# Optimization experiments

Measured on AMD Instinct MI355X. Metric: run time of the kernel, lower is better.

The kernel has to match this reference:

```python
import jax, jax.numpy as jnp
import numpy as np

B, TQ, TK, D, H = 4, 2048, 2048, 512, 8
NEG = -1e9
LN_EPS = 1e-3  # Keras LayerNormalization default


def setup_inputs() -> dict:
    key = jax.random.key(0)
    ks = jax.random.split(key, 5)
    s = 0.02
    return {
        "queries": jax.random.normal(ks[0], (B, TQ, D), jnp.float32),
        "keys_in": jax.random.normal(ks[1], (B, TK, D), jnp.float32),
        "Wq": jax.random.normal(ks[2], (D, D), jnp.float32) * s,
        "bq": jnp.zeros((D,), jnp.float32),
        "Wk": jax.random.normal(ks[3], (D, D), jnp.float32) * s,
        "bk": jnp.zeros((D,), jnp.float32),
        "Wv": jax.random.normal(ks[4], (D, D), jnp.float32) * s,
        "bv": jnp.zeros((D,), jnp.float32),
        "gamma": jnp.ones((D,), jnp.float32),
        "beta": jnp.zeros((D,), jnp.float32),
    }


def reference(queries, keys_in, Wq, bq, Wk, bk, Wv, bv, gamma, beta):
    # Dense projections with relu activation (as in the original layer)
    Q = jax.nn.relu(queries @ Wq + bq)   # [B, Tq, D]
    K = jax.nn.relu(keys_in @ Wk + bk)   # [B, Tk, D]
    V = jax.nn.relu(keys_in @ Wv + bv)   # [B, Tk, D]

    b, tq, d = Q.shape
    tk = K.shape[1]
    dh = d // H
    # split_heads: tf.split(axis=-1)+concat(axis=0) == contiguous feature chunks per head
    Qh = Q.reshape(b, tq, H, dh)
    Kh = K.reshape(b, tk, H, dh)
    Vh = V.reshape(b, tk, H, dh)

    scores = jnp.einsum('bqhd,bkhd->bhqk', Qh, Kh) / jnp.sqrt(jnp.float32(dh))

    # key padding mask derived from per-head K content: sum(|K|) > 0 along dh
    kmask = jnp.sum(jnp.abs(Kh), axis=-1) > 0            # [B, Tk, H]
    kmask = jnp.transpose(kmask, (0, 2, 1))              # [B, H, Tk]
    scores = jnp.where(kmask[:, :, None, :], scores, NEG)

    attn = jax.nn.softmax(scores, axis=-1)               # [B, H, Tq, Tk]

    # query mask: zero out attention rows for all-zero query positions
    qmask = (jnp.sum(jnp.abs(Qh), axis=-1) > 0).astype(attn.dtype)  # [B, Tq, H]
    qmask = jnp.transpose(qmask, (0, 2, 1))              # [B, H, Tq]
    attn = attn * qmask[:, :, :, None]

    out = jnp.einsum('bhqk,bkhd->bqhd', attn, Vh).reshape(b, tq, d)

    # residual + LayerNorm (Keras default: last axis, eps=1e-3)
    res = out + queries
    mu = jnp.mean(res, axis=-1, keepdims=True)
    var = jnp.var(res, axis=-1, keepdims=True)
    return (res - mu) * jax.lax.rsqrt(var + LN_EPS) * gamma + beta
```

## Files before the change

### kernel.cpp

```cpp
#include <hip/hip_runtime.h>
#include <cstdint>

#define BB 4
#define TT 2048
#define DD 512
#define HH 8
#define DH 64
#define NT (TT / 64)
#define LOG2E 1.4426950408889634f

using bf16x8 = __attribute__((ext_vector_type(8))) __bf16;
using f32x4  = __attribute__((ext_vector_type(4))) float;
using f32x16 = __attribute__((ext_vector_type(16))) float;
using us8    = __attribute__((ext_vector_type(8))) unsigned short;
using us4    = __attribute__((ext_vector_type(4))) unsigned short;
using u32x2  = __attribute__((ext_vector_type(2))) unsigned int;

typedef const __attribute__((address_space(1))) unsigned int* as1cp;
typedef __attribute__((address_space(3))) unsigned int* as3p;

__device__ __forceinline__ void gload16(const void* g, void* l) {
  __builtin_amdgcn_global_load_lds((as1cp)(uintptr_t)g,
                                   (as3p)(unsigned int)(uintptr_t)l, 16, 0, 0);
}

__device__ __forceinline__ unsigned short f2bf(float x) {
  unsigned int u = __float_as_uint(x);
  u += 0x7fffu + ((u >> 16) & 1u);
  return (unsigned short)(u >> 16);
}
__device__ __forceinline__ float bf2f(unsigned short u) {
  return __uint_as_float(((unsigned int)u) << 16);
}
__device__ __forceinline__ f32x4 MFMA(bf16x8 a, bf16x8 b, f32x4 c) {
  return __builtin_amdgcn_mfma_f32_16x16x32_bf16(a, b, c, 0, 0, 0);
}
__device__ __forceinline__ f32x16 MFMA32(bf16x8 a, bf16x8 b, f32x16 c) {
  return __builtin_amdgcn_mfma_f32_32x32x16_bf16(a, b, c, 0, 0, 0);
}

#define WAITVM(N) asm volatile("s_waitcnt vmcnt(" #N ")" ::: "memory")
#define RAWBAR() asm volatile("s_barrier" ::: "memory")

__global__ __launch_bounds__(256) void prep_kernel(const float4* __restrict__ q,
                                                   const float4* __restrict__ k,
                                                   us4* __restrict__ qb,
                                                   us4* __restrict__ kb,
                                                   const float* __restrict__ Wq,
                                                   const float* __restrict__ Wk,
                                                   const float* __restrict__ Wv,
                                                   unsigned short* __restrict__ Wt) {
  __shared__ float tile[32][33];
  int id = blockIdx.x;
  if (id < 4096) {
    size_t i = (size_t)id * 256 + threadIdx.x;
    float4 a = q[i];
    us4 o; o[0] = f2bf(a.x); o[1] = f2bf(a.y); o[2] = f2bf(a.z); o[3] = f2bf(a.w);
    qb[i] = o;
    float4 b = k[i];
    us4 p; p[0] = f2bf(b.x); p[1] = f2bf(b.y); p[2] = f2bf(b.z); p[3] = f2bf(b.w);
    kb[i] = p;
  } else {
    int id2 = id - 4096;
    int z = id2 >> 8, rem = id2 & 255;
    const float* W = (z == 0) ? Wq : (z == 1) ? Wk : Wv;
    int k0 = (rem & 15) * 32, n0 = (rem >> 4) * 32;
    int r = threadIdx.x >> 5, c = threadIdx.x & 31;
#pragma unroll
    for (int p = 0; p < 4; ++p)
      tile[r + p * 8][c] = W[(size_t)(k0 + r + p * 8) * DD + n0 + c];
    __syncthreads();
    unsigned short* o = Wt + (size_t)z * DD * DD;
#pragma unroll
    for (int p = 0; p < 4; ++p)
      o[(size_t)(n0 + r + p * 8) * DD + k0 + c] = f2bf(tile[c][r + p * 8]);
  }
}

#define GSTAGE(kt2, pbuf)                                                    \
  {                                                                          \
    int t_ = threadIdx.x;                                                    \
    _Pragma("unroll")                                                        \
    for (int it_ = 0; it_ < 2; ++it_) {                                      \
      int c_ = t_ + it_ * 256;                                               \
      gload16(A  + (size_t)(mb + (c_ >> 2)) * DD + (kt2) * 32 + (c_ & 3) * 8,\
              &As[pbuf][(size_t)c_ * 8]);                                    \
      gload16(Bt + (size_t)(nb + (c_ >> 2)) * DD + (kt2) * 32 + (c_ & 3) * 8,\
              &Bs[pbuf][(size_t)c_ * 8]);                                    \
    }                                                                        \
  }

__global__ __launch_bounds__(256) void gemm_proj(const unsigned short* __restrict__ qb,
                                                 const unsigned short* __restrict__ kb,
                                                 const unsigned short* __restrict__ Wt,
                                                 const float* __restrict__ bq,
                                                 const float* __restrict__ bk,
                                                 const float* __restrict__ bv,
                                                 unsigned short* __restrict__ Qp,
                                                 unsigned short* __restrict__ Kp,
                                                 unsigned short* __restrict__ Vp,
                                                 float* __restrict__ qmask,
                                                 uint2* __restrict__ kbits) {
  int z = blockIdx.z;
  const unsigned short* A  = (z == 0) ? qb : kb;
  const unsigned short* Bt = Wt + (size_t)z * DD * DD;
  const float* bias = (z == 0) ? bq : (z == 1) ? bk : bv;
  unsigned short* out = (z == 0) ? Qp : (z == 1) ? Kp : Vp;
  const float osc = (z == 0) ? 0.125f * LOG2E : 1.0f;

  __shared__ __align__(16) unsigned short As[2][128 * 32];
  __shared__ __align__(16) unsigned short Bs[2][128 * 32];

  int mb = blockIdx.x * 128, nb = blockIdx.y * 128;
  int w = threadIdx.x >> 6, lane = threadIdx.x & 63;
  int l15 = lane & 15, lg = lane >> 4;
  int wr = (w >> 1) * 64, wc = (w & 1) * 64;

  f32x4 acc[4][4] = {};

  GSTAGE(0, 0);
  for (int kt = 0; kt < DD / 32; ++kt) {
    int pb2 = kt & 1;
    if (kt + 1 < DD / 32) {
      GSTAGE(kt + 1, pb2 ^ 1);
      WAITVM(4);
    } else {
      WAITVM(0);
    }
    RAWBAR();

    bf16x8 af[4], bf[4];
#pragma unroll
    for (int m = 0; m < 4; ++m)
      af[m] = *(const bf16x8*)&As[pb2][(wr + m * 16 + l15) * 32 + lg * 8];
#pragma unroll
    for (int n = 0; n < 4; ++n)
      bf[n] = *(const bf16x8*)&Bs[pb2][(wc + n * 16 + l15) * 32 + lg * 8];
#pragma unroll
    for (int m = 0; m < 4; ++m)
#pragma unroll
      for (int n = 0; n < 4; ++n)
        acc[m][n] = MFMA(af[m], bf[n], acc[m][n]);

    if (kt + 1 < DD / 32) RAWBAR();
  }

  float rs_[16];
#pragma unroll
  for (int j = 0; j < 16; ++j) rs_[j] = 0.f;
#pragma unroll
  for (int m = 0; m < 4; ++m)
#pragma unroll
    for (int n = 0; n < 4; ++n)
#pragma unroll
      for (int i = 0; i < 4; ++i) {
        int row = mb + wr + m * 16 + lg * 4 + i;
        int col = nb + wc + n * 16 + l15;
        float v = fmaxf(acc[m][n][i] + bias[col], 0.f);
        rs_[m * 4 + i] += v;
        out[(size_t)row * DD + col] = f2bf(v * osc);
      }

  if (z < 2) {
#pragma unroll
    for (int j = 0; j < 16; ++j) {
      rs_[j] += __shfl_xor(rs_[j], 1);
      rs_[j] += __shfl_xor(rs_[j], 2);
      rs_[j] += __shfl_xor(rs_[j], 4);
      rs_[j] += __shfl_xor(rs_[j], 8);
    }
    int gr0 = mb + wr;
    int b = gr0 >> 11, tpos0 = gr0 & (TT - 1);
    int h = (nb + wc) >> 6;
    int bh = b * HH + h;
    if (z == 0) {
      if (l15 == 0) {
#pragma unroll
        for (int m = 0; m < 4; ++m)
#pragma unroll
          for (int i = 0; i < 4; ++i) {
            int tpos = tpos0 + m * 16 + lg * 4 + i;
            qmask[(size_t)bh * TT + tpos] = (rs_[m * 4 + i] > 0.f) ? 1.f : 0.f;
          }
      }
    } else {
      unsigned long long wloc = 0;
#pragma unroll
      for (int m = 0; m < 4; ++m)
#pragma unroll
        for (int i = 0; i < 4; ++i)
          if (rs_[m * 4 + i] > 0.f)
            wloc |= 1ull << (m * 16 + lg * 4 + i);
      wloc |= __shfl_xor(wloc, 16);
      wloc |= __shfl_xor(wloc, 32);
      if (lane == 0)
        kbits[bh * NT + (tpos0 >> 6)] =
            make_uint2((unsigned int)wloc, (unsigned int)(wloc >> 32));
    }
  }
}

__global__ __launch_bounds__(256) void post_v(const unsigned short* __restrict__ Vp,
                                              unsigned short* __restrict__ Vt) {
  __shared__ unsigned short tile[64][72];
  int id = blockIdx.x;
  int b = id >> 8, k0 = (id & 31) * 64, d0 = ((id >> 5) & 7) * 64;
  int t = threadIdx.x;
  int r = t >> 3, c8 = (t & 7) * 8;
#pragma unroll
  for (int p = 0; p < 2; ++p) {
    int row = r + p * 32;
    us8 v = *(const us8*)&Vp[(size_t)(b * TT + k0 + row) * DD + d0 + c8];
#pragma unroll
    for (int j = 0; j < 8; ++j) tile[row][c8 + j] = v[j];
  }
  __syncthreads();
#pragma unroll
  for (int p = 0; p < 2; ++p) {
    int dr = r + p * 32;
    us8 o;
#pragma unroll
    for (int j = 0; j < 8; ++j) o[j] = tile[c8 + j][dr];
    *(us8*)&Vt[((size_t)b * DD + d0 + dr) * TT + k0 + c8] = o;
  }
}

#define STAGE(tt, pbuf)                                                      \
  {                                                                          \
    int c0_ = threadIdx.x;                                                   \
    _Pragma("unroll")                                                        \
    for (int it_ = 0; it_ < 2; ++it_) {                                      \
      int c_ = c0_ + it_ * 256;                                              \
      int r_ = c_ >> 3, j_ = c_ & 7;                                         \
      int js_ = j_ ^ (r_ & 7);                                               \
      int kr_ = (r_ & ~12) | ((r_ & 4) << 1) | ((r_ & 8) >> 1);              \
      gload16(kg + (size_t)((tt) * 64 + kr_) * DD + js_ * 8,                 \
              &KsBuf[pbuf][(size_t)c_ * 8]);                                 \
      gload16(vg + (size_t)r_ * TT + (tt) * 64 + js_ * 8,                    \
              &VsBuf[pbuf][(size_t)c_ * 8]);                                 \
    }                                                                        \
  }

__global__ __launch_bounds__(256) void attn_kernel(
    const unsigned short* __restrict__ Qp,
    const unsigned short* __restrict__ Kp,
    const unsigned short* __restrict__ Vt,
    const uint2* __restrict__ kbits,
    const float* __restrict__ qmask,
    unsigned short* __restrict__ O) {
  __shared__ __align__(16) unsigned short KsBuf[2][64 * 64];
  __shared__ __align__(16) unsigned short VsBuf[2][64 * 64];

  const int w = threadIdx.x >> 6;
  const int lane = threadIdx.x & 63;
  const int l31 = lane & 31, h2 = lane >> 5;

  int flat = blockIdx.x;
  int wg = (flat & 7) * 64 + (flat >> 3);
  int qt = wg & 15, bh = wg >> 4;
  int h = bh & 7, b = bh >> 3;
  int q0 = qt * 128 + w * 32;

  const unsigned short* qbase =
      Qp + ((size_t)(b * TT + q0 + l31)) * DD + h * DH + h2 * 8;
  bf16x8 qf[4];
#pragma unroll
  for (int kd = 0; kd < 4; ++kd) qf[kd] = *(const bf16x8*)(qbase + kd * 16);

  const unsigned short* kg = Kp + ((size_t)b * TT) * DD + h * DH;
  const unsigned short* vg = Vt + ((size_t)(b * DD + h * DH)) * TT;
  const uint2* kb_ptr = kbits + (size_t)bh * NT;

  f32x16 oat0 = {}, oat1 = {};
  float l_i = 0.f;

  STAGE(0, 0);

  for (int t = 0; t < NT; ++t) {
    int pb = t & 1;
    if (t + 1 < NT) {
      STAGE(t + 1, pb ^ 1);
      WAITVM(4);
    } else {
      WAITVM(0);
    }
    RAWBAR();

    const unsigned short* ksb = &KsBuf[pb][0];
    const unsigned short* vsb = &VsBuf[pb][0];

    bf16x8 kf0[4], kf1[4];
#pragma unroll
    for (int kd = 0; kd < 4; ++kd) {
      int x = ((kd * 2 + h2) ^ (l31 & 7)) << 3;
      kf0[kd] = *(const bf16x8*)&ksb[l31 * 64 + x];
      kf1[kd] = *(const bf16x8*)&ksb[(32 + l31) * 64 + x];
    }
    f32x16 s0 = {}, s1 = {};
    __builtin_amdgcn_s_setprio(1);
#pragma unroll
    for (int kd = 0; kd < 4; ++kd) s0 = MFMA32(kf0[kd], qf[kd], s0);
#pragma unroll
    for (int kd = 0; kd < 4; ++kd) s1 = MFMA32(kf1[kd], qf[kd], s1);
    __builtin_amdgcn_s_setprio(0);

    bf16x8 vf0[4], vf1[4];
#pragma unroll
    for (int ks = 0; ks < 4; ++ks) {
      int x = ((ks * 2 + h2) ^ (l31 & 7)) << 3;
      vf0[ks] = *(const bf16x8*)&vsb[l31 * 64 + x];
      vf1[ks] = *(const bf16x8*)&vsb[(32 + l31) * 64 + x];
    }

    uint2 kw = kb_ptr[t];
    if ((kw.x & kw.y) != 0xffffffffu) {
#pragma unroll
      for (int r = 0; r < 16; ++r) {
        int sh = ((r >> 3) << 4) + (h2 << 3) + (r & 7);
        if (!((kw.x >> sh) & 1)) s0[r] = -1e30f;
        if (!((kw.y >> sh) & 1)) s1[r] = -1e30f;
      }
    }

    float a0 = 0.f, a1 = 0.f, a2 = 0.f, a3 = 0.f;
#pragma unroll
    for (int r = 0; r < 8; ++r)  { float p = exp2f(s0[r]); s0[r] = p; a0 += p; }
#pragma unroll
    for (int r = 8; r < 16; ++r) { float p = exp2f(s0[r]); s0[r] = p; a1 += p; }
#pragma unroll
    for (int r = 0; r < 8; ++r)  { float p = exp2f(s1[r]); s1[r] = p; a2 += p; }
#pragma unroll
    for (int r = 8; r < 16; ++r) { float p = exp2f(s1[r]); s1[r] = p; a3 += p; }
    l_i += (a0 + a1) + (a2 + a3);

    bf16x8 pbf[4];
#pragma unroll
    for (int j = 0; j < 8; ++j) {
      pbf[0][j] = (__bf16)s0[j];
      pbf[1][j] = (__bf16)s0[8 + j];
      pbf[2][j] = (__bf16)s1[j];
      pbf[3][j] = (__bf16)s1[8 + j];
    }

    __builtin_amdgcn_s_setprio(1);
#pragma unroll
    for (int ks = 0; ks < 4; ++ks) {
      oat0 = MFMA32(vf0[ks], pbf[ks], oat0);
      oat1 = MFMA32(vf1[ks], pbf[ks], oat1);
    }
    __builtin_amdgcn_s_setprio(0);

    if (t + 1 < NT) RAWBAR();
  }

  u32x2 sr = __builtin_amdgcn_permlane32_swap(__float_as_uint(l_i),
                                              __float_as_uint(l_i), false, false);
  float l = __uint_as_float(sr[0]) + __uint_as_float(sr[1]);
  float qm = qmask[(size_t)bh * TT + q0 + l31];
  float sc = qm / fmaxf(l, 1e-30f);
  unsigned short* ob = O + ((size_t)(b * TT + q0 + l31)) * DD + h * DH + h2 * 4;
#pragma unroll
  for (int qq = 0; qq < 4; ++qq) {
    us4 w0, w1;
#pragma unroll
    for (int i = 0; i < 4; ++i) {
      w0[i] = f2bf(oat0[4 * qq + i] * sc);
      w1[i] = f2bf(oat1[4 * qq + i] * sc);
    }
    *(us4*)(ob + 8 * qq) = w0;
    *(us4*)(ob + 32 + 8 * qq) = w1;
  }
}

__global__ __launch_bounds__(256) void ln_kernel(const unsigned short* __restrict__ O,
                                                 const float* __restrict__ qin,
                                                 const float* __restrict__ gamma,
                                                 const float* __restrict__ beta,
                                                 float* __restrict__ out) {
  int row = blockIdx.x * 4 + (threadIdx.x >> 6);
  int lane = threadIdx.x & 63;
  size_t base = (size_t)row * DD + lane * 8;
  us8 o = *(const us8*)(O + base);
  const float4* q4 = (const float4*)(qin + base);
  float4 c = q4[0], d2 = q4[1];
  float qv[8] = {c.x, c.y, c.z, c.w, d2.x, d2.y, d2.z, d2.w};
  float v[8];
#pragma unroll
  for (int j = 0; j < 8; ++j) v[j] = bf2f(o[j]) + qv[j];
  float s = 0.f, s2 = 0.f;
#pragma unroll
  for (int j = 0; j < 8; ++j) { s += v[j]; s2 += v[j] * v[j]; }
#pragma unroll
  for (int xm = 1; xm < 64; xm <<= 1) {
    s += __shfl_xor(s, xm);
    s2 += __shfl_xor(s2, xm);
  }
  float mu = s * (1.0f / DD);
  float var = s2 * (1.0f / DD) - mu * mu;
  float rs = rsqrtf(var + 1e-3f);
  const float* g = gamma + lane * 8;
  const float* bb = beta + lane * 8;
  float* ob = out + base;
#pragma unroll
  for (int j = 0; j < 8; ++j) ob[j] = (v[j] - mu) * rs * g[j] + bb[j];
}

extern "C" void kernel_launch(void* const* d_in, const int* in_sizes, int n_in,
                              void* d_out, int out_size, void* d_ws, size_t ws_size,
                              hipStream_t stream) {
  (void)in_sizes; (void)n_in; (void)out_size; (void)ws_size;
  const float* queries = (const float*)d_in[0];
  const float* keys_in = (const float*)d_in[1];
  const float* Wq = (const float*)d_in[2];
  const float* bq = (const float*)d_in[3];
  const float* Wk = (const float*)d_in[4];
  const float* bk = (const float*)d_in[5];
  const float* Wv = (const float*)d_in[6];
  const float* bv = (const float*)d_in[7];
  const float* gamma = (const float*)d_in[8];
  const float* beta  = (const float*)d_in[9];
  float* out = (float*)d_out;

  char* ws = (char*)d_ws;
  unsigned short* qb = (unsigned short*)(ws);
  unsigned short* kb = (unsigned short*)(ws + (8ull << 20));
  unsigned short* Obf = (unsigned short*)(ws);
  unsigned short* Qp = (unsigned short*)(ws + (16ull << 20));
  unsigned short* Kp = (unsigned short*)(ws + (24ull << 20));
  unsigned short* Vp = (unsigned short*)(ws + (32ull << 20));
  unsigned short* Vt = (unsigned short*)(ws + (40ull << 20));
  unsigned short* Wt = (unsigned short*)(ws + (48ull << 20));
  float* qmaskp = (float*)(ws + (50ull << 20));
  uint2* kbitsp = (uint2*)(ws + (50ull << 20) + (512ull << 10));

  prep_kernel<<<4864, 256, 0, stream>>>((const float4*)queries, (const float4*)keys_in,
                                        (us4*)qb, (us4*)kb, Wq, Wk, Wv, Wt);
  gemm_proj<<<dim3(64, 4, 3), 256, 0, stream>>>(qb, kb, Wt, bq, bk, bv,
                                                Qp, Kp, Vp, qmaskp, kbitsp);
  post_v<<<1024, 256, 0, stream>>>(Vp, Vt);
  attn_kernel<<<512, 256, 0, stream>>>(Qp, Kp, Vt, kbitsp, qmaskp, Obf);
  ln_kernel<<<2048, 256, 0, stream>>>(Obf, queries, gamma, beta, out);
}
```

Measured before the change: 195.0 us.

## Fuse fp32-to-bf16 conversion and V transpose into projection GEMM, unroll attention loop

The projection GEMM now loads fp32 activations straight into LDS and converts them to bf16 while building fragments. This removes the separate activation conversion pass and its intermediate buffers. The V projection epilogue writes transposed bf16 directly, which removes the post_v kernel. The attention loop is unrolled by two with pointer increments, and the softmax row sum is computed with an MFMA against a ones vector instead of scalar adds. In exchange, the GEMM uses twice the LDS for the A tile and does more conversion work per fragment, and the transposed V stores are strided 8-byte writes.

```diff
diff --git a/kernel.cpp b/kernel.cpp
--- a/kernel.cpp
+++ b/kernel.cpp
@@ -42,73 +42,61 @@
 #define WAITVM(N) asm volatile("s_waitcnt vmcnt(" #N ")" ::: "memory")
 #define RAWBAR() asm volatile("s_barrier" ::: "memory")
 
-__global__ __launch_bounds__(256) void prep_kernel(const float4* __restrict__ q,
-                                                   const float4* __restrict__ k,
-                                                   us4* __restrict__ qb,
-                                                   us4* __restrict__ kb,
-                                                   const float* __restrict__ Wq,
-                                                   const float* __restrict__ Wk,
-                                                   const float* __restrict__ Wv,
-                                                   unsigned short* __restrict__ Wt) {
+__global__ __launch_bounds__(256) void prep_w(const float* __restrict__ Wq,
+                                              const float* __restrict__ Wk,
+                                              const float* __restrict__ Wv,
+                                              unsigned short* __restrict__ Wt) {
   __shared__ float tile[32][33];
   int id = blockIdx.x;
-  if (id < 4096) {
-    size_t i = (size_t)id * 256 + threadIdx.x;
-    float4 a = q[i];
-    us4 o; o[0] = f2bf(a.x); o[1] = f2bf(a.y); o[2] = f2bf(a.z); o[3] = f2bf(a.w);
-    qb[i] = o;
-    float4 b = k[i];
-    us4 p; p[0] = f2bf(b.x); p[1] = f2bf(b.y); p[2] = f2bf(b.z); p[3] = f2bf(b.w);
-    kb[i] = p;
-  } else {
-    int id2 = id - 4096;
-    int z = id2 >> 8, rem = id2 & 255;
-    const float* W = (z == 0) ? Wq : (z == 1) ? Wk : Wv;
-    int k0 = (rem & 15) * 32, n0 = (rem >> 4) * 32;
-    int r = threadIdx.x >> 5, c = threadIdx.x & 31;
-#pragma unroll
-    for (int p = 0; p < 4; ++p)
-      tile[r + p * 8][c] = W[(size_t)(k0 + r + p * 8) * DD + n0 + c];
-    __syncthreads();
-    unsigned short* o = Wt + (size_t)z * DD * DD;
-#pragma unroll
-    for (int p = 0; p < 4; ++p)
-      o[(size_t)(n0 + r + p * 8) * DD + k0 + c] = f2bf(tile[c][r + p * 8]);
-  }
-}
-
-#define GSTAGE(kt2, pbuf)                                                    \
-  {                                                                          \
-    int t_ = threadIdx.x;                                                    \
-    _Pragma("unroll")                                                        \
-    for (int it_ = 0; it_ < 2; ++it_) {                                      \
-      int c_ = t_ + it_ * 256;                                               \
-      gload16(A  + (size_t)(mb + (c_ >> 2)) * DD + (kt2) * 32 + (c_ & 3) * 8,\
-              &As[pbuf][(size_t)c_ * 8]);                                    \
-      gload16(Bt + (size_t)(nb + (c_ >> 2)) * DD + (kt2) * 32 + (c_ & 3) * 8,\
-              &Bs[pbuf][(size_t)c_ * 8]);                                    \
-    }                                                                        \
-  }
-
-__global__ __launch_bounds__(256) void gemm_proj(const unsigned short* __restrict__ qb,
-                                                 const unsigned short* __restrict__ kb,
+  int z = id >> 8, rem = id & 255;
+  const float* W = (z == 0) ? Wq : (z == 1) ? Wk : Wv;
+  int k0 = (rem & 15) * 32, n0 = (rem >> 4) * 32;
+  int r = threadIdx.x >> 5, c = threadIdx.x & 31;
+#pragma unroll
+  for (int p = 0; p < 4; ++p)
+    tile[r + p * 8][c] = W[(size_t)(k0 + r + p * 8) * DD + n0 + c];
+  __syncthreads();
+  unsigned short* o = Wt + (size_t)z * DD * DD;
+#pragma unroll
+  for (int p = 0; p < 4; ++p)
+    o[(size_t)(n0 + r + p * 8) * DD + k0 + c] = f2bf(tile[c][r + p * 8]);
+}
+
+#define GSTAGE(kt2, pbuf)                                                     \
+  {                                                                           \
+    int t_ = threadIdx.x;                                                     \
+    _Pragma("unroll")                                                         \
+    for (int it_ = 0; it_ < 4; ++it_) {                                       \
+      int c_ = t_ + it_ * 256;             \
+      gload16(A + (size_t)(mb + (c_ >> 3)) * DD + (kt2) * 32 + (c_ & 7) * 4,  \
+              &Asf[pbuf][(size_t)c_ * 4]);                                    \
+    }                                                                         \
+    _Pragma("unroll")                                                         \
+    for (int it_ = 0; it_ < 2; ++it_) {                                       \
+      int c_ = t_ + it_ * 256;             \
+      gload16(Bt + (size_t)(nb + (c_ >> 2)) * DD + (kt2) * 32 + (c_ & 3) * 8, \
+              &Bs[pbuf][(size_t)c_ * 8]);                                     \
+    }                                                                         \
+  }
+
+__global__ __launch_bounds__(256) void gemm_proj(const float* __restrict__ queries,
+                                                 const float* __restrict__ keys_in,
                                                  const unsigned short* __restrict__ Wt,
                                                  const float* __restrict__ bq,
                                                  const float* __restrict__ bk,
                                                  const float* __restrict__ bv,
                                                  unsigned short* __restrict__ Qp,
                                                  unsigned short* __restrict__ Kp,
-                                                 unsigned short* __restrict__ Vp,
+                                                 unsigned short* __restrict__ Vt,
                                                  float* __restrict__ qmask,
                                                  uint2* __restrict__ kbits) {
   int z = blockIdx.z;
-  const unsigned short* A  = (z == 0) ? qb : kb;
+  const float* A = (z == 0) ? queries : keys_in;
   const unsigned short* Bt = Wt + (size_t)z * DD * DD;
   const float* bias = (z == 0) ? bq : (z == 1) ? bk : bv;
-  unsigned short* out = (z == 0) ? Qp : (z == 1) ? Kp : Vp;
   const float osc = (z == 0) ? 0.125f * LOG2E : 1.0f;
 
-  __shared__ __align__(16) unsigned short As[2][128 * 32];
+  __shared__ __align__(16) float Asf[2][128 * 32];
   __shared__ __align__(16) unsigned short Bs[2][128 * 32];
 
   int mb = blockIdx.x * 128, nb = blockIdx.y * 128;
@@ -123,7 +111,7 @@
     int pb2 = kt & 1;
     if (kt + 1 < DD / 32) {
       GSTAGE(kt + 1, pb2 ^ 1);
-      WAITVM(4);
+      WAITVM(6);
     } else {
       WAITVM(0);
     }
@@ -131,8 +119,16 @@
 
     bf16x8 af[4], bf[4];
 #pragma unroll
-    for (int m = 0; m < 4; ++m)
-      af[m] = *(const bf16x8*)&As[pb2][(wr + m * 16 + l15) * 32 + lg * 8];
+    for (int m = 0; m < 4; ++m) {
+      int base = (wr + m * 16 + l15) * 32 + lg * 8;
+      f32x4 lo = *(const f32x4*)&Asf[pb2][base];
+      f32x4 hi = *(const f32x4*)&Asf[pb2][base + 4];
+#pragma unroll
+      for (int j = 0; j < 4; ++j) {
+        af[m][j] = (__bf16)lo[j];
+        af[m][4 + j] = (__bf16)hi[j];
+      }
+    }
 #pragma unroll
     for (int n = 0; n < 4; ++n)
       bf[n] = *(const bf16x8*)&Bs[pb2][(wc + n * 16 + l15) * 32 + lg * 8];
@@ -148,20 +144,21 @@
   float rs_[16];
 #pragma unroll
   for (int j = 0; j < 16; ++j) rs_[j] = 0.f;
-#pragma unroll
-  for (int m = 0; m < 4; ++m)
-#pragma unroll
-    for (int n = 0; n < 4; ++n)
-#pragma unroll
-      for (int i = 0; i < 4; ++i) {
-        int row = mb + wr + m * 16 + lg * 4 + i;
-        int col = nb + wc + n * 16 + l15;
-        float v = fmaxf(acc[m][n][i] + bias[col], 0.f);
-        rs_[m * 4 + i] += v;
-        out[(size_t)row * DD + col] = f2bf(v * osc);
-      }
 
   if (z < 2) {
+    unsigned short* out = (z == 0) ? Qp : Kp;
+#pragma unroll
+    for (int m = 0; m < 4; ++m)
+#pragma unroll
+      for (int n = 0; n < 4; ++n)
+#pragma unroll
+        for (int i = 0; i < 4; ++i) {
+          int row = mb + wr + m * 16 + lg * 4 + i;
+          int col = nb + wc + n * 16 + l15;
+          float v = fmaxf(acc[m][n][i] + bias[col], 0.f);
+          rs_[m * 4 + i] += v;
+          out[(size_t)row * DD + col] = f2bf(v * osc);
+        }
 #pragma unroll
     for (int j = 0; j < 16; ++j) {
       rs_[j] += __shfl_xor(rs_[j], 1);
@@ -197,35 +194,24 @@
         kbits[bh * NT + (tpos0 >> 6)] =
             make_uint2((unsigned int)wloc, (unsigned int)(wloc >> 32));
     }
-  }
-}
-
-__global__ __launch_bounds__(256) void post_v(const unsigned short* __restrict__ Vp,
-                                              unsigned short* __restrict__ Vt) {
-  __shared__ unsigned short tile[64][72];
-  int id = blockIdx.x;
-  int b = id >> 8, k0 = (id & 31) * 64, d0 = ((id >> 5) & 7) * 64;
-  int t = threadIdx.x;
-  int r = t >> 3, c8 = (t & 7) * 8;
-#pragma unroll
-  for (int p = 0; p < 2; ++p) {
-    int row = r + p * 32;
-    us8 v = *(const us8*)&Vp[(size_t)(b * TT + k0 + row) * DD + d0 + c8];
-#pragma unroll
-    for (int j = 0; j < 8; ++j) tile[row][c8 + j] = v[j];
-  }
-  __syncthreads();
-#pragma unroll
-  for (int p = 0; p < 2; ++p) {
-    int dr = r + p * 32;
-    us8 o;
-#pragma unroll
-    for (int j = 0; j < 8; ++j) o[j] = tile[c8 + j][dr];
-    *(us8*)&Vt[((size_t)b * DD + d0 + dr) * TT + k0 + c8] = o;
-  }
-}
-
-#define STAGE(tt, pbuf)                                                      \
+  } else {
+    int b = mb >> 11;
+    int tok0 = (mb & (TT - 1)) + wr + lg * 4;
+#pragma unroll
+    for (int m = 0; m < 4; ++m)
+#pragma unroll
+      for (int n = 0; n < 4; ++n) {
+        int col = nb + wc + n * 16 + l15;
+        us4 pk;
+#pragma unroll
+        for (int i = 0; i < 4; ++i)
+          pk[i] = f2bf(fmaxf(acc[m][n][i] + bias[col], 0.f));
+        *(us4*)&Vt[((size_t)b * DD + col) * TT + tok0 + m * 16] = pk;
+      }
+  }
+}
+
+#define STAGE(kgt, vgt, pbuf)                                                \
   {                                                                          \
     int c0_ = threadIdx.x;                                                   \
     _Pragma("unroll")                                                        \
@@ -234,11 +220,79 @@
       int r_ = c_ >> 3, j_ = c_ & 7;                                         \
       int js_ = j_ ^ (r_ & 7);                                               \
       int kr_ = (r_ & ~12) | ((r_ & 4) << 1) | ((r_ & 8) >> 1);              \
-      gload16(kg + (size_t)((tt) * 64 + kr_) * DD + js_ * 8,                 \
+      gload16((kgt) + (size_t)kr_ * DD + js_ * 8,                            \
               &KsBuf[pbuf][(size_t)c_ * 8]);                                 \
-      gload16(vg + (size_t)r_ * TT + (tt) * 64 + js_ * 8,                    \
+      gload16((vgt) + (size_t)r_ * TT + js_ * 8,                             \
               &VsBuf[pbuf][(size_t)c_ * 8]);                                 \
     }                                                                        \
+  }
+
+#define ATTN_TILE(pbuf, do_stage)                                            \
+  {                                                                          \
+    if (do_stage) {                                                          \
+      STAGE(kgt, vgt, pbuf ^ 1);                                             \
+      kgt += 64 * DD;                                                        \
+      vgt += 64;                                                             \
+      WAITVM(4);                                                             \
+    } else {                                                                 \
+      WAITVM(0);                                                             \
+    }                                                                        \
+    RAWBAR();                                                                \
+    const unsigned short* ksb = &KsBuf[pbuf][0];                             \
+    const unsigned short* vsb = &VsBuf[pbuf][0];                             \
+    bf16x8 kf0[4], kf1[4];                                                   \
+    _Pragma("unroll")                                                        \
+    for (int kd = 0; kd < 4; ++kd) {                                         \
+      int x = ((kd * 2 + h2) ^ (l31 & 7)) << 3;                              \
+      kf0[kd] = *(const bf16x8*)&ksb[l31 * 64 + x];                          \
+      kf1[kd] = *(const bf16x8*)&ksb[(32 + l31) * 64 + x];                   \
+    }                                                                        \
+    f32x16 s0 = {}, s1 = {};                                                 \
+    __builtin_amdgcn_s_setprio(1);                                           \
+    _Pragma("unroll")                                                        \
+    for (int kd = 0; kd < 4; ++kd) s0 = MFMA32(kf0[kd], qf[kd], s0);         \
+    _Pragma("unroll")                                                        \
+    for (int kd = 0; kd < 4; ++kd) s1 = MFMA32(kf1[kd], qf[kd], s1);         \
+    __builtin_amdgcn_s_setprio(0);                                           \
+    bf16x8 vf0[4], vf1[4];                                                   \
+    _Pragma("unroll")                                                        \
+    for (int ks = 0; ks < 4; ++ks) {                                         \
+      int x = ((ks * 2 + h2) ^ (l31 & 7)) << 3;                              \
+      vf0[ks] = *(const bf16x8*)&vsb[l31 * 64 + x];                          \
+      vf1[ks] = *(const bf16x8*)&vsb[(32 + l31) * 64 + x];                   \
+    }                                                                        \
+    uint2 kw = *kbt;                                                         \
+    ++kbt;                                                                   \
+    if ((kw.x & kw.y) != 0xffffffffu) {                                      \
+      _Pragma("unroll")                                                      \
+      for (int r = 0; r < 16; ++r) {                                         \
+        int sh = ((r >> 3) << 4) + (h2 << 3) + (r & 7);                      \
+        if (!((kw.x >> sh) & 1)) s0[r] = -1e30f;                             \
+        if (!((kw.y >> sh) & 1)) s1[r] = -1e30f;                             \
+      }                                                                      \
+    }                                                                        \
+    _Pragma("unroll")                                                        \
+    for (int r = 0; r < 16; ++r) {                                           \
+      s0[r] = exp2f(s0[r]);                                                  \
+      s1[r] = exp2f(s1[r]);                                                  \
+    }                                                                        \
+    bf16x8 pbf[4];                                                           \
+    _Pragma("unroll")                                                        \
+    for (int j = 0; j < 8; ++j) {                                            \
+      pbf[0][j] = (__bf16)s0[j];                                             \
+      pbf[1][j] = (__bf16)s0[8 + j];                                         \
+      pbf[2][j] = (__bf16)s1[j];                                             \
+      pbf[3][j] = (__bf16)s1[8 + j];                                         \
+    }                                                                        \
+    __builtin_amdgcn_s_setprio(1);                                           \
+    _Pragma("unroll")                                                        \
+    for (int ks = 0; ks < 4; ++ks) {                                         \
+      oat0 = MFMA32(vf0[ks], pbf[ks], oat0);                                 \
+      oat1 = MFMA32(vf1[ks], pbf[ks], oat1);                                 \
+      lacc = MFMA32(ones, pbf[ks], lacc);                                    \
+    }                                                                        \
+    __builtin_amdgcn_s_setprio(0);                                           \
+    if (do_stage) RAWBAR();                                                  \
   }
 
 __global__ __launch_bounds__(256) void attn_kernel(
@@ -267,92 +321,29 @@
 #pragma unroll
   for (int kd = 0; kd < 4; ++kd) qf[kd] = *(const bf16x8*)(qbase + kd * 16);
 
-  const unsigned short* kg = Kp + ((size_t)b * TT) * DD + h * DH;
-  const unsigned short* vg = Vt + ((size_t)(b * DD + h * DH)) * TT;
-  const uint2* kb_ptr = kbits + (size_t)bh * NT;
-
-  f32x16 oat0 = {}, oat1 = {};
-  float l_i = 0.f;
-
-  STAGE(0, 0);
-
-  for (int t = 0; t < NT; ++t) {
-    int pb = t & 1;
-    if (t + 1 < NT) {
-      STAGE(t + 1, pb ^ 1);
-      WAITVM(4);
-    } else {
-      WAITVM(0);
-    }
-    RAWBAR();
-
-    const unsigned short* ksb = &KsBuf[pb][0];
-    const unsigned short* vsb = &VsBuf[pb][0];
-
-    bf16x8 kf0[4], kf1[4];
-#pragma unroll
-    for (int kd = 0; kd < 4; ++kd) {
-      int x = ((kd * 2 + h2) ^ (l31 & 7)) << 3;
-      kf0[kd] = *(const bf16x8*)&ksb[l31 * 64 + x];
-      kf1[kd] = *(const bf16x8*)&ksb[(32 + l31) * 64 + x];
-    }
-    f32x16 s0 = {}, s1 = {};
-    __builtin_amdgcn_s_setprio(1);
-#pragma unroll
-    for (int kd = 0; kd < 4; ++kd) s0 = MFMA32(kf0[kd], qf[kd], s0);
-#pragma unroll
-    for (int kd = 0; kd < 4; ++kd) s1 = MFMA32(kf1[kd], qf[kd], s1);
-    __builtin_amdgcn_s_setprio(0);
-
-    bf16x8 vf0[4], vf1[4];
-#pragma unroll
-    for (int ks = 0; ks < 4; ++ks) {
-      int x = ((ks * 2 + h2) ^ (l31 & 7)) << 3;
-      vf0[ks] = *(const bf16x8*)&vsb[l31 * 64 + x];
-      vf1[ks] = *(const bf16x8*)&vsb[(32 + l31) * 64 + x];
-    }
-
-    uint2 kw = kb_ptr[t];
-    if ((kw.x & kw.y) != 0xffffffffu) {
-#pragma unroll
-      for (int r = 0; r < 16; ++r) {
-        int sh = ((r >> 3) << 4) + (h2 << 3) + (r & 7);
-        if (!((kw.x >> sh) & 1)) s0[r] = -1e30f;
-        if (!((kw.y >> sh) & 1)) s1[r] = -1e30f;
-      }
-    }
-
-    float a0 = 0.f, a1 = 0.f, a2 = 0.f, a3 = 0.f;
-#pragma unroll
-    for (int r = 0; r < 8; ++r)  { float p = exp2f(s0[r]); s0[r] = p; a0 += p; }
-#pragma unroll
-    for (int r = 8; r < 16; ++r) { float p = exp2f(s0[r]); s0[r] = p; a1 += p; }
-#pragma unroll
-    for (int r = 0; r < 8; ++r)  { float p = exp2f(s1[r]); s1[r] = p; a2 += p; }
-#pragma unroll
-    for (int r = 8; r < 16; ++r) { float p = exp2f(s1[r]); s1[r] = p; a3 += p; }
-    l_i += (a0 + a1) + (a2 + a3);
-
-    bf16x8 pbf[4];
-#pragma unroll
-    for (int j = 0; j < 8; ++j) {
-      pbf[0][j] = (__bf16)s0[j];
-      pbf[1][j] = (__bf16)s0[8 + j];
-      pbf[2][j] = (__bf16)s1[j];
-      pbf[3][j] = (__bf16)s1[8 + j];
-    }
-
-    __builtin_amdgcn_s_setprio(1);
-#pragma unroll
-    for (int ks = 0; ks < 4; ++ks) {
-      oat0 = MFMA32(vf0[ks], pbf[ks], oat0);
-      oat1 = MFMA32(vf1[ks], pbf[ks], oat1);
-    }
-    __builtin_amdgcn_s_setprio(0);
-
-    if (t + 1 < NT) RAWBAR();
-  }
-
+  const unsigned short* kgt = Kp + ((size_t)b * TT) * DD + h * DH;
+  const unsigned short* vgt = Vt + ((size_t)(b * DD + h * DH)) * TT;
+  const uint2* kbt = kbits + (size_t)bh * NT;
+
+  bf16x8 ones;
+#pragma unroll
+  for (int j = 0; j < 8; ++j) ones[j] = (__bf16)1.0f;
+
+  f32x16 oat0 = {}, oat1 = {}, lacc = {};
+
+  STAGE(kgt, vgt, 0);
+  kgt += 64 * DD;
+  vgt += 64;
+
+#pragma unroll 1
+  for (int t = 0; t < NT - 2; t += 2) {
+    ATTN_TILE(0, 1)
+    ATTN_TILE(1, 1)
+  }
+  ATTN_TILE(0, 1)
+  ATTN_TILE(1, 0)
+
+  float l_i = lacc[0];
   u32x2 sr = __builtin_amdgcn_permlane32_swap(__float_as_uint(l_i),
                                               __float_as_uint(l_i), false, false);
   float l = __uint_as_float(sr[0]) + __uint_as_float(sr[1]);
@@ -422,22 +413,17 @@
   float* out = (float*)d_out;
 
   char* ws = (char*)d_ws;
-  unsigned short* qb = (unsigned short*)(ws);
-  unsigned short* kb = (unsigned short*)(ws + (8ull << 20));
   unsigned short* Obf = (unsigned short*)(ws);
-  unsigned short* Qp = (unsigned short*)(ws + (16ull << 20));
-  unsigned short* Kp = (unsigned short*)(ws + (24ull << 20));
-  unsigned short* Vp = (unsigned short*)(ws + (32ull << 20));
-  unsigned short* Vt = (unsigned short*)(ws + (40ull << 20));
-  unsigned short* Wt = (unsigned short*)(ws + (48ull << 20));
+  unsigned short* Qp  = (unsigned short*)(ws + (16ull << 20));
+  unsigned short* Kp  = (unsigned short*)(ws + (24ull << 20));
+  unsigned short* Vt  = (unsigned short*)(ws + (32ull << 20));
+  unsigned short* Wt  = (unsigned short*)(ws + (48ull << 20));
   float* qmaskp = (float*)(ws + (50ull << 20));
   uint2* kbitsp = (uint2*)(ws + (50ull << 20) + (512ull << 10));
 
-  prep_kernel<<<4864, 256, 0, stream>>>((const float4*)queries, (const float4*)keys_in,
-                                        (us4*)qb, (us4*)kb, Wq, Wk, Wv, Wt);
-  gemm_proj<<<dim3(64, 4, 3), 256, 0, stream>>>(qb, kb, Wt, bq, bk, bv,
-                                                Qp, Kp, Vp, qmaskp, kbitsp);
-  post_v<<<1024, 256, 0, stream>>>(Vp, Vt);
+  prep_w<<<768, 256, 0, stream>>>(Wq, Wk, Wv, Wt);
+  gemm_proj<<<dim3(64, 4, 3), 256, 0, stream>>>(queries, keys_in, Wt, bq, bk, bv,
+                                                Qp, Kp, Vt, qmaskp, kbitsp);
   attn_kernel<<<512, 256, 0, stream>>>(Qp, Kp, Vt, kbitsp, qmaskp, Obf);
   ln_kernel<<<2048, 256, 0, stream>>>(Obf, queries, gamma, beta, out);
 }
```

Result: slower. 204.1 us (+4.7%).
